# Optimization experiments

Measured on AMD Instinct MI355X. Metric: run time of the kernel, lower is better.

The kernel has to match this reference:

```python
import jax, jax.numpy as jnp
import numpy as np


def setup_inputs() -> dict:
    key = jax.random.key(0)
    k1, k2 = jax.random.split(key)
    B, C, H, W, D = 2, 1, 128, 128, 128
    image = jax.random.normal(k1, (B, C, H, W, D), dtype=jnp.float32)
    # dense displacement field in voxel units (typical registration magnitudes)
    ddf = jax.random.normal(k2, (B, 3, H, W, D), dtype=jnp.float32) * 3.0
    return {"image": image, "ddf": ddf}


def _warp(image, ddf):
    """Trilinear grid_sample warp, padding_mode='zeros', align_corners=True.

    Equivalent to MONAI Warp(mode=1, padding_mode='zeros'): the reference grid
    plus DDF gives absolute voxel coordinates; torch's normalization to [-1,1]
    with align_corners=True followed by grid_sample maps exactly back to these
    voxel coordinates, so we sample directly in voxel space.
    """
    B, C, H, W, D = image.shape
    dt = image.dtype
    mesh = jnp.stack(
        jnp.meshgrid(
            jnp.arange(H, dtype=dt),
            jnp.arange(W, dtype=dt),
            jnp.arange(D, dtype=dt),
            indexing="ij",
        ),
        axis=-1,
    )  # (H, W, D, 3)
    coords = mesh[None] + jnp.moveaxis(ddf, 1, -1)  # (B, H, W, D, 3) voxel coords

    c0f = jnp.floor(coords)
    frac = coords - c0f                      # (B, H, W, D, 3)
    c0 = c0f.astype(jnp.int32)
    sizes = jnp.array([H, W, D], dtype=jnp.int32)
    strides = jnp.array([W * D, D, 1], dtype=jnp.int32)

    N = H * W * D
    img_flat = image.reshape(B, C, N)
    out = jnp.zeros((B, C, N), dtype=dt)
    # 8 trilinear taps; zeros padding => out-of-range taps contribute 0
    for dx in (0, 1):
        for dy in (0, 1):
            for dz in (0, 1):
                off = jnp.array([dx, dy, dz], dtype=jnp.int32)
                idx = c0 + off                                   # (B,H,W,D,3)
                wsel = jnp.where(off == 1, frac, 1.0 - frac)
                w = wsel[..., 0] * wsel[..., 1] * wsel[..., 2]   # (B,H,W,D)
                valid = jnp.all((idx >= 0) & (idx < sizes), axis=-1)
                idxc = jnp.clip(idx, 0, sizes - 1)
                lin = jnp.sum(idxc * strides, axis=-1).reshape(B, N)
                vals = jax.vmap(lambda im, li: im[:, li])(img_flat, lin)  # (B,C,N)
                out = out + vals * (w * valid.astype(dt)).reshape(B, 1, N)
    return out.reshape(B, C, H, W, D)


def reference(image, ddf):
    return _warp(image, ddf)
```

## Files before the change

kernel.cpp:

```cpp
#include <hip/hip_runtime.h>
#include <hip/hip_fp16.h>


constexpr int H = 128, W = 128, D = 128;
constexpr int N = H * W * D;
constexpr int B = 2;
constexpr int HA = 8;
constexpr int RS = 32;
constexpr int RN = RS * RS * RS;

typedef float fvec4 __attribute__((ext_vector_type(4)));

__global__ __launch_bounds__(1024, 8) void warp_tile_kernel(
    const float* __restrict__ image,
    const float* __restrict__ ddf,
    float* __restrict__ out)
{
    __shared__ __half tile[RN];

    int bid = blockIdx.x;
    int b  = bid >> 9;
    int t3 = bid & 511;
    int tx0 = ((t3 >> 6) & 7) << 4;
    int ty0 = ((t3 >> 3) & 7) << 4;
    int tz0 = (t3 & 7) << 4;
    int ox = tx0 - HA, oy = ty0 - HA, oz = tz0 - HA;

    const float* img = image + ((size_t)b << 21);
    int t = threadIdx.x;

    int zq = (t & 3) << 2;
    int ly = (t >> 2) & 15;
    int lx = t >> 6;
    int vx = tx0 + lx, vy = ty0 + ly, vz = tz0 + zq;
    int lin0 = (vx << 14) + (vy << 7) + vz;

    const float* ddfb = ddf + (size_t)b * 3 * N;
    fvec4 dx4 = *(const fvec4*)(ddfb + lin0);
    fvec4 dy4 = *(const fvec4*)(ddfb + lin0 + N);
    fvec4 dz4 = *(const fvec4*)(ddfb + lin0 + 2 * N);

    fvec4 sa[4], sb[4];
    int rows[4], zos[4];
#pragma unroll
    for (int c = 0; c < 4; ++c) {
        int s   = c * 1024 + t;
        int row = s >> 2;
        int zo  = (s & 3) << 3;
        rows[c] = row; zos[c] = zo;
        int gx = ox + (row >> 5);
        int gy = oy + (row & 31);
        int gz = oz + zo;
        bool ok = ((unsigned)gx < 128u) & ((unsigned)gy < 128u) & ((unsigned)gz < 121u);
        const float* p = img + (gx << 14) + (gy << 7) + gz;
        fvec4 z4 = {0.f, 0.f, 0.f, 0.f};
        sa[c] = ok ? *(const fvec4*)p       : z4;
        sb[c] = ok ? *(const fvec4*)(p + 4) : z4;
    }
    unsigned short* tp = (unsigned short*)tile;
#pragma unroll
    for (int c = 0; c < 4; ++c) {
        __half2 h0 = __floats2half2_rn(sa[c].x, sa[c].y);
        __half2 h1 = __floats2half2_rn(sa[c].z, sa[c].w);
        __half2 h2 = __floats2half2_rn(sb[c].x, sb[c].y);
        __half2 h3 = __floats2half2_rn(sb[c].z, sb[c].w);
        uint4 pk;
        pk.x = *(unsigned int*)&h0;
        pk.y = *(unsigned int*)&h1;
        pk.z = *(unsigned int*)&h2;
        pk.w = *(unsigned int*)&h3;
        *(uint4*)(tp + rows[c] * 32 + zos[c]) = pk;
    }
    __syncthreads();

    float* outb = out + ((size_t)b << 21);
    const unsigned int* cells = (const unsigned int*)tile;
    float dxp[4] = {dx4.x, dx4.y, dx4.z, dx4.w};
    float dyp[4] = {dy4.x, dy4.y, dy4.z, dy4.w};
    float dzp[4] = {dz4.x, dz4.y, dz4.z, dz4.w};
    float res[4];

#pragma unroll
    for (int i = 0; i < 4; ++i) {
        float x = (float)vx + dxp[i];
        float y = (float)vy + dyp[i];
        float z = (float)(vz + i) + dzp[i];

        float xf = floorf(x), yf = floorf(y), zf = floorf(z);
        float fx = x - xf, fy = y - yf, fz = z - zf;
        int x0 = (int)xf, y0 = (int)yf, z0 = (int)zf;
        int rx = x0 - ox, ry = y0 - oy, rz = z0 - oz;

        float acc;
        if ((unsigned)rx <= 30u && (unsigned)ry <= 30u && (unsigned)rz <= 30u) {
            int rowc = ((rx << 5) + ry) << 4;
            int c  = rowc + (rz >> 1);
            int sh = (rz & 1) << 4;
            unsigned l00 = cells[c];
            unsigned h00 = cells[c + 1];
            unsigned l01 = cells[c + 16];
            unsigned h01 = cells[c + 17];
            unsigned l10 = cells[c + 512];
            unsigned h10 = cells[c + 513];
            unsigned l11 = cells[c + 528];
            unsigned h11 = cells[c + 529];

            float az0 = 1.f - fz;
            float zz[4];
            unsigned los[4] = {l00, l01, l10, l11};
            unsigned his[4] = {h00, h01, h10, h11};
#pragma unroll
            for (int p2 = 0; p2 < 4; ++p2) {
                unsigned long long v = ((unsigned long long)his[p2] << 32) | los[p2];
                unsigned pr = (unsigned)(v >> sh);
                __half2 hp = *(__half2*)&pr;
                float2 f2 = __half22float2(hp);
                zz[p2] = az0 * f2.x + fz * f2.y;
            }
            float ay0 = 1.f - fy;
            acc = (1.f - fx) * (ay0 * zz[0] + fy * zz[1]) +
                  fx         * (ay0 * zz[2] + fy * zz[3]);
        } else {
            int x1 = x0 + 1, y1 = y0 + 1, z1 = z0 + 1;
            bool vx0 = (unsigned)x0 < (unsigned)H;
            bool vx1 = (unsigned)x1 < (unsigned)H;
            bool vy0 = (unsigned)y0 < (unsigned)W;
            bool vy1 = (unsigned)y1 < (unsigned)W;
            bool vz0 = (unsigned)z0 < (unsigned)D;
            bool vz1 = (unsigned)z1 < (unsigned)D;
            float ax0 = vx0 ? (1.0f - fx) : 0.0f;
            float ax1 = vx1 ? fx          : 0.0f;
            float ay0 = vy0 ? (1.0f - fy) : 0.0f;
            float ay1 = vy1 ? fy          : 0.0f;
            float az0 = vz0 ? (1.0f - fz) : 0.0f;
            float az1 = vz1 ? fz          : 0.0f;
            int cx0 = vx0 ? x0 : 0;
            int cx1 = vx1 ? x1 : 0;
            int cy0 = vy0 ? y0 : 0;
            int cy1 = vy1 ? y1 : 0;
            int cz0 = vz0 ? z0 : 0;
            int cz1 = vz1 ? z1 : 0;
            int rx0 = cx0 << 14, rx1 = cx1 << 14;
            int ry0 = cy0 << 7,  ry1 = cy1 << 7;
            float v000 = img[rx0 + ry0 + cz0];
            float v001 = img[rx0 + ry0 + cz1];
            float v010 = img[rx0 + ry1 + cz0];
            float v011 = img[rx0 + ry1 + cz1];
            float v100 = img[rx1 + ry0 + cz0];
            float v101 = img[rx1 + ry0 + cz1];
            float v110 = img[rx1 + ry1 + cz0];
            float v111 = img[rx1 + ry1 + cz1];
            acc = ax0 * (ay0 * (az0 * v000 + az1 * v001) +
                         ay1 * (az0 * v010 + az1 * v011)) +
                  ax1 * (ay0 * (az0 * v100 + az1 * v101) +
                         ay1 * (az0 * v110 + az1 * v111));
        }
        res[i] = acc;
    }
    fvec4 r4 = {res[0], res[1], res[2], res[3]};
    __builtin_nontemporal_store(r4, (fvec4*)(outb + lin0));
}

extern "C" void kernel_launch(void* const* d_in, const int* in_sizes, int n_in,
                              void* d_out, int out_size, void* d_ws, size_t ws_size,
                              hipStream_t stream) {
    const float* image = (const float*)d_in[0];
    const float* ddf   = (const float*)d_in[1];
    float* out = (float*)d_out;

    warp_tile_kernel<<<B * 512, 1024, 0, stream>>>(image, ddf, out);
}
```

Before: 112.0 us.

## Process two z-adjacent tiles per block with prefetch overlapping compute

Each block now handles two consecutive 16-voxel z tiles, halving the grid to 512 blocks. Global loads for the second tile's halo and displacement field are issued before and during the first tile's compute, so load latency overlaps with sampling work. The cost is extra registers to hold the prefetched data, more barriers, and fewer blocks in flight. Halo reloads are not shared between the two tiles.

```diff
diff --git a/kernel.cpp b/kernel.cpp
--- a/kernel.cpp
+++ b/kernel.cpp
@@ -11,69 +11,45 @@
 
 typedef float fvec4 __attribute__((ext_vector_type(4)));
 
-__global__ __launch_bounds__(1024, 8) void warp_tile_kernel(
-    const float* __restrict__ image,
-    const float* __restrict__ ddf,
-    float* __restrict__ out)
-{
-    __shared__ __half tile[RN];
-
-    int bid = blockIdx.x;
-    int b  = bid >> 9;
-    int t3 = bid & 511;
-    int tx0 = ((t3 >> 6) & 7) << 4;
-    int ty0 = ((t3 >> 3) & 7) << 4;
-    int tz0 = (t3 & 7) << 4;
-    int ox = tx0 - HA, oy = ty0 - HA, oz = tz0 - HA;
-
-    const float* img = image + ((size_t)b << 21);
-    int t = threadIdx.x;
-
-    int zq = (t & 3) << 2;
-    int ly = (t >> 2) & 15;
-    int lx = t >> 6;
-    int vx = tx0 + lx, vy = ty0 + ly, vz = tz0 + zq;
-    int lin0 = (vx << 14) + (vy << 7) + vz;
-
-    const float* ddfb = ddf + (size_t)b * 3 * N;
-    fvec4 dx4 = *(const fvec4*)(ddfb + lin0);
-    fvec4 dy4 = *(const fvec4*)(ddfb + lin0 + N);
-    fvec4 dz4 = *(const fvec4*)(ddfb + lin0 + 2 * N);
-
-    fvec4 sa[4], sb[4];
-    int rows[4], zos[4];
-#pragma unroll
-    for (int c = 0; c < 4; ++c) {
-        int s   = c * 1024 + t;
-        int row = s >> 2;
-        int zo  = (s & 3) << 3;
-        rows[c] = row; zos[c] = zo;
-        int gx = ox + (row >> 5);
-        int gy = oy + (row & 31);
-        int gz = oz + zo;
-        bool ok = ((unsigned)gx < 128u) & ((unsigned)gy < 128u) & ((unsigned)gz < 121u);
-        const float* p = img + (gx << 14) + (gy << 7) + gz;
-        fvec4 z4 = {0.f, 0.f, 0.f, 0.f};
-        sa[c] = ok ? *(const fvec4*)p       : z4;
-        sb[c] = ok ? *(const fvec4*)(p + 4) : z4;
-    }
-    unsigned short* tp = (unsigned short*)tile;
-#pragma unroll
-    for (int c = 0; c < 4; ++c) {
-        __half2 h0 = __floats2half2_rn(sa[c].x, sa[c].y);
-        __half2 h1 = __floats2half2_rn(sa[c].z, sa[c].w);
-        __half2 h2 = __floats2half2_rn(sb[c].x, sb[c].y);
-        __half2 h3 = __floats2half2_rn(sb[c].z, sb[c].w);
-        uint4 pk;
-        pk.x = *(unsigned int*)&h0;
-        pk.y = *(unsigned int*)&h1;
-        pk.z = *(unsigned int*)&h2;
-        pk.w = *(unsigned int*)&h3;
-        *(uint4*)(tp + rows[c] * 32 + zos[c]) = pk;
-    }
-    __syncthreads();
-
-    float* outb = out + ((size_t)b << 21);
+__device__ __forceinline__ void stage_load(const float* __restrict__ img,
+    int ox, int oy, int oz, int t, int c, fvec4& A, fvec4& Bv)
+{
+    int s   = c * 1024 + t;
+    int row = s >> 2;
+    int zo  = (s & 3) << 3;
+    int gx = ox + (row >> 5);
+    int gy = oy + (row & 31);
+    int gz = oz + zo;
+    bool ok = ((unsigned)gx < 128u) & ((unsigned)gy < 128u) & ((unsigned)gz < 121u);
+    const float* p = img + (gx << 14) + (gy << 7) + gz;
+    fvec4 z4 = {0.f, 0.f, 0.f, 0.f};
+    A  = ok ? *(const fvec4*)p       : z4;
+    Bv = ok ? *(const fvec4*)(p + 4) : z4;
+}
+
+__device__ __forceinline__ void stage_write(__half* __restrict__ tile,
+    int t, int c, fvec4 A, fvec4 Bv)
+{
+    int s   = c * 1024 + t;
+    int row = s >> 2;
+    int zo  = (s & 3) << 3;
+    __half2 h0 = __floats2half2_rn(A.x, A.y);
+    __half2 h1 = __floats2half2_rn(A.z, A.w);
+    __half2 h2 = __floats2half2_rn(Bv.x, Bv.y);
+    __half2 h3 = __floats2half2_rn(Bv.z, Bv.w);
+    uint4 pk;
+    pk.x = *(unsigned int*)&h0;
+    pk.y = *(unsigned int*)&h1;
+    pk.z = *(unsigned int*)&h2;
+    pk.w = *(unsigned int*)&h3;
+    *(uint4*)((unsigned short*)tile + row * 32 + zo) = pk;
+}
+
+__device__ __forceinline__ void compute_tile(const __half* __restrict__ tile,
+    const float* __restrict__ img, float* __restrict__ outb,
+    int vx, int vy, int vz, int lin0, int ox, int oy, int oz,
+    fvec4 dx4, fvec4 dy4, fvec4 dz4)
+{
     const unsigned int* cells = (const unsigned int*)tile;
     float dxp[4] = {dx4.x, dx4.y, dx4.z, dx4.w};
     float dyp[4] = {dy4.x, dy4.y, dy4.z, dy4.w};
@@ -96,19 +72,12 @@
             int rowc = ((rx << 5) + ry) << 4;
             int c  = rowc + (rz >> 1);
             int sh = (rz & 1) << 4;
-            unsigned l00 = cells[c];
-            unsigned h00 = cells[c + 1];
-            unsigned l01 = cells[c + 16];
-            unsigned h01 = cells[c + 17];
-            unsigned l10 = cells[c + 512];
-            unsigned h10 = cells[c + 513];
-            unsigned l11 = cells[c + 528];
-            unsigned h11 = cells[c + 529];
-
+            unsigned los[4] = {cells[c],       cells[c + 16],
+                               cells[c + 512], cells[c + 528]};
+            unsigned his[4] = {cells[c + 1],   cells[c + 17],
+                               cells[c + 513], cells[c + 529]};
             float az0 = 1.f - fz;
             float zz[4];
-            unsigned los[4] = {l00, l01, l10, l11};
-            unsigned his[4] = {h00, h01, h10, h11};
 #pragma unroll
             for (int p2 = 0; p2 < 4; ++p2) {
                 unsigned long long v = ((unsigned long long)his[p2] << 32) | los[p2];
@@ -161,6 +130,72 @@
     __builtin_nontemporal_store(r4, (fvec4*)(outb + lin0));
 }
 
+__global__ __launch_bounds__(1024, 8) void warp_pair_kernel(
+    const float* __restrict__ image,
+    const float* __restrict__ ddf,
+    float* __restrict__ out)
+{
+    __shared__ __half tile[RN];
+
+    int bid = blockIdx.x;
+    int b = bid >> 8;
+    int p = bid & 255;
+    int tx0 = ((p >> 5) & 7) << 4;
+    int ty0 = ((p >> 2) & 7) << 4;
+    int tzA = (p & 3) << 5;
+    int tzB = tzA + 16;
+    int ox = tx0 - HA, oy = ty0 - HA;
+    int ozA = tzA - HA, ozB = tzB - HA;
+
+    const float* img  = image + ((size_t)b << 21);
+    const float* ddfb = ddf + (size_t)b * 3 * N;
+    float* outb = out + ((size_t)b << 21);
+    int t = threadIdx.x;
+
+    int zq = (t & 3) << 2;
+    int ly = (t >> 2) & 15;
+    int lx = t >> 6;
+    int vx = tx0 + lx, vy = ty0 + ly;
+    int vzA = tzA + zq, vzB = tzB + zq;
+    int linA = (vx << 14) + (vy << 7) + vzA;
+    int linB = linA + 16;
+
+    fvec4 adx = *(const fvec4*)(ddfb + linA);
+    fvec4 ady = *(const fvec4*)(ddfb + linA + N);
+    fvec4 adz = *(const fvec4*)(ddfb + linA + 2 * N);
+
+    fvec4 s0, s1, s2, s3, u0, u1, u2, u3;
+    stage_load(img, ox, oy, ozA, t, 0, s0, u0);
+    stage_load(img, ox, oy, ozA, t, 1, s1, u1);
+    stage_load(img, ox, oy, ozA, t, 2, s2, u2);
+    stage_load(img, ox, oy, ozA, t, 3, s3, u3);
+    stage_write(tile, t, 0, s0, u0);
+    stage_write(tile, t, 1, s1, u1);
+    stage_write(tile, t, 2, s2, u2);
+    stage_write(tile, t, 3, s3, u3);
+
+    fvec4 bdx = *(const fvec4*)(ddfb + linB);
+    fvec4 bdy = *(const fvec4*)(ddfb + linB + N);
+    fvec4 bdz = *(const fvec4*)(ddfb + linB + 2 * N);
+    stage_load(img, ox, oy, ozB, t, 0, s0, u0);
+    stage_load(img, ox, oy, ozB, t, 1, s1, u1);
+
+    __syncthreads();
+    compute_tile(tile, img, outb, vx, vy, vzA, linA, ox, oy, ozA, adx, ady, adz);
+
+    stage_load(img, ox, oy, ozB, t, 2, s2, u2);
+    stage_load(img, ox, oy, ozB, t, 3, s3, u3);
+
+    __syncthreads();
+    stage_write(tile, t, 0, s0, u0);
+    stage_write(tile, t, 1, s1, u1);
+    stage_write(tile, t, 2, s2, u2);
+    stage_write(tile, t, 3, s3, u3);
+    __syncthreads();
+
+    compute_tile(tile, img, outb, vx, vy, vzB, linB, ox, oy, ozB, bdx, bdy, bdz);
+}
+
 extern "C" void kernel_launch(void* const* d_in, const int* in_sizes, int n_in,
                               void* d_out, int out_size, void* d_ws, size_t ws_size,
                               hipStream_t stream) {
@@ -168,5 +203,5 @@
     const float* ddf   = (const float*)d_in[1];
     float* out = (float*)d_out;
 
-    warp_tile_kernel<<<B * 512, 1024, 0, stream>>>(image, ddf, out);
-}
+    warp_pair_kernel<<<512, 1024, 0, stream>>>(image, ddf, out);
+}
```

Result: slower. 130.4 us (+16.5%).
